# Performance work log

Measured on AMD Instinct MI355X. Metric: run time of the kernel, lower is better.

The kernel has to match this reference:

```python
import jax, jax.numpy as jnp
import numpy as np

N_HOPS = 2
LEAKY_SLOPE = 0.2
EPS = 1e-12


def setup_inputs() -> dict:
    key = jax.random.key(0)
    k1, k2, k3, k4, k5, k6 = jax.random.split(key, 6)
    N, R, C, E = 100000, 50, 64, 1000000
    return {
        "entity_emb": jax.random.normal(k1, (N, C), dtype=jnp.float32) * 0.1,
        "relation_emb": jax.random.normal(k2, (R, C), dtype=jnp.float32) * 0.1,
        "fc_w": jax.random.normal(k3, (C, 2 * C), dtype=jnp.float32) * 0.1,  # torch Linear weight [out, in]
        "fc_b": jax.random.normal(k4, (C,), dtype=jnp.float32) * 0.1,
        "edge_index": jax.random.randint(k5, (2, E), 0, N, dtype=jnp.int64),
        "edge_type": jax.random.randint(k6, (E,), 0, R, dtype=jnp.int64),
    }


def reference(entity_emb, relation_emb, fc_w, fc_b, edge_index, edge_type):
    """RGAT.forward with mess_dropout=False: n_hops of relational-attention
    gather -> leakyrelu -> scatter_softmax(head) -> scatter_sum -> residual -> L2 normalize."""
    N = entity_emb.shape[0]
    head, tail = edge_index[0], edge_index[1]
    rel_e = relation_emb[edge_type]  # [E, C]

    def agg(emb):
        a_input = jnp.concatenate([emb[head], emb[tail]], axis=-1)  # [E, 2C]
        h = a_input @ fc_w.T + fc_b                                  # fc(a_input): [E, C]
        e = jnp.sum(h * rel_e, axis=-1)                              # [E]
        e = jnp.where(e > 0, e, LEAKY_SLOPE * e)                     # leakyrelu(0.2)
        # scatter_softmax over head segments (numerically stable)
        m = jax.ops.segment_max(e, head, num_segments=N)             # [N]
        ex = jnp.exp(e - m[head])
        denom = jax.ops.segment_sum(ex, head, num_segments=N)        # [N]
        w = ex / denom[head]                                         # [E]
        agg_emb = jax.ops.segment_sum(emb[tail] * w[:, None], head, num_segments=N)
        agg_emb = agg_emb + emb                                      # residual
        return agg_emb

    emb = entity_emb
    for _ in range(N_HOPS):
        emb = agg(emb)
        # F.normalize(emb): L2 along dim=1 with eps clamp
        nrm = jnp.sqrt(jnp.sum(emb * emb, axis=-1, keepdims=True))
        emb = emb / jnp.maximum(nrm, EPS)
    return emb
```

## Files before the change

kernel.cpp:

```cpp
#include <hip/hip_runtime.h>

#define C 64
#define RMAX 50
#define LEAKY 0.2f
#define CAP 48

__device__ __forceinline__ float bf2f(unsigned short u) {
  return __uint_as_float(((unsigned)u) << 16);
}
__device__ __forceinline__ unsigned short f2bf(float x) {
  unsigned u = __float_as_uint(x);
  return (unsigned short)((u + 0x7FFFu + ((u >> 16) & 1u)) >> 16);
}

__device__ __forceinline__ int wave_isbf(const void* ent) {
  const unsigned* w = (const unsigned*)ent;
  const int lane = threadIdx.x & 63;
  int ok = 0;
#pragma unroll
  for (int i = 0; i < 4; ++i) {
    unsigned lo = w[lane + 64 * i] & 0xFFFFu;
    float a = fabsf(__uint_as_float(lo << 16));
    ok += (lo == 0u || (a >= 1e-9f && a <= 1e9f)) ? 1 : 0;
  }
#pragma unroll
  for (int d = 1; d < 64; d <<= 1) ok += __shfl_xor(ok, d, 64);
  return ok >= 224;
}
__device__ __forceinline__ int wave_is64(const int* p) {
  const int lane = threadIdx.x & 63;
  int z = (p[2 * lane + 1] == 0) ? 1 : 0;
#pragma unroll
  for (int d = 1; d < 64; d <<= 1) z += __shfl_xor(z, d, 64);
  return z >= 62;
}
__device__ __forceinline__ float loadF(const void* p, int i, int isbf) {
  return isbf ? bf2f(((const unsigned short*)p)[i]) : ((const float*)p)[i];
}

__global__ void uvc_kernel(const void* __restrict__ rel,
                           const void* __restrict__ fcw,
                           const void* __restrict__ fcb,
                           float* __restrict__ U, float* __restrict__ V,
                           float* __restrict__ cvec) {
  const int isbf = wave_isbf(rel);
  const int r = blockIdx.x;
  const int i = threadIdx.x;
  float acc = 0.f;
  for (int o = 0; o < C; ++o)
    acc += loadF(rel, r * C + o, isbf) * loadF(fcw, o * (2 * C) + i, isbf);
  if (i < C) U[r * C + i] = acc;
  else       V[r * C + (i - C)] = acc;
  if (i < C) {
    float p = loadF(rel, r * C + i, isbf) * loadF(fcb, i, isbf);
#pragma unroll
    for (int d = 1; d < 64; d <<= 1) p += __shfl_xor(p, d, 64);
    if (i == 0) cvec[r] = p;
  }
}

__global__ void fillb_kernel(const int* __restrict__ eidx, const int* __restrict__ etype,
                             int* __restrict__ cnt, int* __restrict__ packed,
                             int E, int N, int Rc) {
  const int is64 = wave_is64(eidx);
  const int et64 = wave_is64(etype);
  const int base = (blockIdx.x * blockDim.x + threadIdx.x) * 4;
  int h[4], t[4], r[4];
#pragma unroll
  for (int k = 0; k < 4; ++k) {
    const int e = base + k;
    if (e < E) {
      h[k] = is64 ? eidx[2 * e] : eidx[e];
      t[k] = is64 ? eidx[2 * E + 2 * e] : eidx[E + e];
      r[k] = et64 ? etype[2 * e] : etype[e];
    }
  }
  int pos[4];
#pragma unroll
  for (int k = 0; k < 4; ++k) {
    const int e = base + k;
    if (e < E) {
      if ((unsigned)h[k] >= (unsigned)N) h[k] = 0;
      pos[k] = atomicAdd(&cnt[h[k]], 1);
    }
  }
#pragma unroll
  for (int k = 0; k < 4; ++k) {
    const int e = base + k;
    if (e < E && pos[k] < CAP) {
      int tt = t[k]; if ((unsigned)tt >= (unsigned)N) tt = 0;
      int rr = r[k]; if ((unsigned)rr >= (unsigned)Rc) rr = 0;
      packed[h[k] * CAP + pos[k]] = tt | (rr << 20);
    }
  }
}

__global__ void histo_kernel(const int* __restrict__ cnt, int* __restrict__ hist, int N) {
  __shared__ int histS[65];
  const int tid = threadIdx.x;
  for (int k = tid; k < 65; k += 1024) histS[k] = 0;
  __syncthreads();
  const int i = blockIdx.x * 1024 + tid;
  if (i < N) {
    int b = cnt[i]; if (b > 64) b = 64;
    atomicAdd(&histS[b], 1);
  }
  __syncthreads();
  for (int k = tid; k < 65; k += 1024)
    if (histS[k]) atomicAdd(&hist[k], histS[k]);
}

__global__ void order_kernel(const int* __restrict__ cnt, const int* __restrict__ hist,
                             int* __restrict__ bincur, int* __restrict__ order, int N) {
  __shared__ int binstart[66];
  __shared__ int lh[65];
  __shared__ int lbase[65];
  const int tid = threadIdx.x;
  for (int k = tid; k < 65; k += 1024) { binstart[k] = hist[k]; lh[k] = 0; }
  __syncthreads();
  if (tid == 0) {
    int run = 0;
    for (int k = 0; k < 65; ++k) { int t = binstart[k]; binstart[k] = run; run += t; }
    binstart[65] = run;
  }
  __syncthreads();
  const int i = blockIdx.x * 1024 + tid;
  int b = 0, lpos = 0;
  if (i < N) {
    b = cnt[i]; if (b > 64) b = 64;
    lpos = atomicAdd(&lh[b], 1);
  }
  __syncthreads();
  if (tid < 65) lbase[tid] = lh[tid] ? atomicAdd(&bincur[tid], lh[tid]) : 0;
  __syncthreads();
  if (i < N) {
    int dst = binstart[b] + lbase[b] + lpos;
    if ((unsigned)dst < (unsigned)N) order[dst] = i;
  }
}

__device__ __forceinline__ void unpack8(uint4 u, float4& a, float4& b) {
  a.x = __uint_as_float(u.x << 16); a.y = __uint_as_float(u.x & 0xFFFF0000u);
  a.z = __uint_as_float(u.y << 16); a.w = __uint_as_float(u.y & 0xFFFF0000u);
  b.x = __uint_as_float(u.z << 16); b.y = __uint_as_float(u.z & 0xFFFF0000u);
  b.z = __uint_as_float(u.w << 16); b.w = __uint_as_float(u.w & 0xFFFF0000u);
}

template <bool IN_EXT, bool OUT_EXT>
__global__ __launch_bounds__(256) void hop_kernel(
    const void* __restrict__ emb_in_v, void* __restrict__ emb_out_v,
    const int* __restrict__ cnt, const int* __restrict__ packed,
    const float* __restrict__ Ug, const float* __restrict__ Vg,
    const float* __restrict__ cg, const int* __restrict__ order,
    const void* __restrict__ ent_det, int N, int Rc) {
  const int isbf = wave_isbf(ent_det);
  const int l = threadIdx.x & 7;
  const int slot = blockIdx.x * 32 + (threadIdx.x >> 3);
  if (slot >= N) return;
  const int n = order[slot];

  auto loadRow = [&](int row, float4& a, float4& b) {
    if (IN_EXT && !isbf) {
      const float4* q = (const float4*)((const float*)emb_in_v + (size_t)row * C);
      a = q[2 * l]; b = q[2 * l + 1];
    } else {
      uint4 u = ((const uint4*)emb_in_v)[(size_t)row * 8 + l];
      unpack8(u, a, b);
    }
  };

  const int start = n * CAP;
  int deg = cnt[n];
  if (deg > CAP) deg = CAP;
  if (deg < 0) deg = 0;

  float4 enA, enB;
  loadRow(n, enA, enB);

  float sum = 0.f;
  float4 accA = {0.f, 0.f, 0.f, 0.f}, accB = {0.f, 0.f, 0.f, 0.f};

  float4 etA, etB, uuA, uuB, vvA, vvB;
  float cb = 0.f;
  auto issue = [&](unsigned pkv) {
    int t = (int)(pkv & 0xFFFFFu); if (t >= N) t = 0;
    int r = (int)(pkv >> 20);      if (r >= Rc) r = 0;
    loadRow(t, etA, etB);
    const float4* uq = (const float4*)&Ug[r * C + l * 8];
    const float4* vq = (const float4*)&Vg[r * C + l * 8];
    uuA = uq[0]; uuB = uq[1];
    vvA = vq[0]; vvB = vq[1];
    cb = cg[r];
  };
  if (deg > 0) issue((unsigned)packed[start]);
  int pknext = (deg > 1) ? packed[start + 1] : 0;

  for (int jj = 0; jj < deg; ++jj) {
    const float4 cetA = etA, cetB = etB;
    const float4 cuuA = uuA, cuuB = uuB, cvvA = vvA, cvvB = vvB;
    const float ccb = cb;
    if (jj + 1 < deg) issue((unsigned)pknext);
    if (jj + 2 < deg) pknext = packed[start + jj + 2];

    float p = cuuA.x * enA.x + cuuA.y * enA.y + cuuA.z * enA.z + cuuA.w * enA.w
            + cuuB.x * enB.x + cuuB.y * enB.y + cuuB.z * enB.z + cuuB.w * enB.w
            + cvvA.x * cetA.x + cvvA.y * cetA.y + cvvA.z * cetA.z + cvvA.w * cetA.w
            + cvvB.x * cetB.x + cvvB.y * cetB.y + cvvB.z * cetB.z + cvvB.w * cetB.w;
    p += __shfl_xor(p, 1); p += __shfl_xor(p, 2); p += __shfl_xor(p, 4);
    float s = p + ccb;
    s = s > 0.f ? s : LEAKY * s;
    const float wgt = __expf(fminf(s, 50.f));
    sum += wgt;
    accA.x += wgt * cetA.x; accA.y += wgt * cetA.y;
    accA.z += wgt * cetA.z; accA.w += wgt * cetA.w;
    accB.x += wgt * cetB.x; accB.y += wgt * cetB.y;
    accB.z += wgt * cetB.z; accB.w += wgt * cetB.w;
  }

  const float inv = (deg > 0) ? 1.0f / sum : 0.f;
  float4 oA, oB;
  oA.x = accA.x * inv + enA.x; oA.y = accA.y * inv + enA.y;
  oA.z = accA.z * inv + enA.z; oA.w = accA.w * inv + enA.w;
  oB.x = accB.x * inv + enB.x; oB.y = accB.y * inv + enB.y;
  oB.z = accB.z * inv + enB.z; oB.w = accB.w * inv + enB.w;

  float ss = oA.x * oA.x + oA.y * oA.y + oA.z * oA.z + oA.w * oA.w
           + oB.x * oB.x + oB.y * oB.y + oB.z * oB.z + oB.w * oB.w;
  ss += __shfl_xor(ss, 1); ss += __shfl_xor(ss, 2); ss += __shfl_xor(ss, 4);
  const float sc = 1.0f / fmaxf(sqrtf(ss), 1e-12f);
  oA.x *= sc; oA.y *= sc; oA.z *= sc; oA.w *= sc;
  oB.x *= sc; oB.y *= sc; oB.z *= sc; oB.w *= sc;

  if (OUT_EXT && !isbf) {
    float4* q = (float4*)((float*)emb_out_v + (size_t)n * C);
    q[2 * l] = oA; q[2 * l + 1] = oB;
  } else {
    uint4 u;
    u.x = (unsigned)f2bf(oA.x) | ((unsigned)f2bf(oA.y) << 16);
    u.y = (unsigned)f2bf(oA.z) | ((unsigned)f2bf(oA.w) << 16);
    u.z = (unsigned)f2bf(oB.x) | ((unsigned)f2bf(oB.y) << 16);
    u.w = (unsigned)f2bf(oB.z) | ((unsigned)f2bf(oB.w) << 16);
    ((uint4*)emb_out_v)[(size_t)n * 8 + l] = u;
  }
}

extern "C" void kernel_launch(void* const* d_in, const int* in_sizes, int n_in,
                              void* d_out, int out_size, void* d_ws, size_t ws_size,
                              hipStream_t stream) {
  const void* ent  = d_in[0];
  const void* rel  = d_in[1];
  const void* fcw  = d_in[2];
  const void* fcb  = d_in[3];
  const int* eidx  = (const int*)d_in[4];
  const int* etype = (const int*)d_in[5];

  const int N  = in_sizes[0] / C;
  const int R0 = in_sizes[1] / C;
  const int Rc = R0 < RMAX ? R0 : RMAX;
  const int E  = in_sizes[5];
  const int nbN = (N + 1023) / 1024;
  (void)n_in; (void)out_size; (void)ws_size;

  char* ws = (char*)d_ws;
  size_t off = 0;
  auto alloc = [&](size_t bytes) -> void* {
    void* p = ws + off;
    off = (off + bytes + 255) & ~(size_t)255;
    return p;
  };
  int*   cnt    = (int*)alloc(((size_t)N + 256) * 4);
  int*   hist   = cnt + N;
  int*   bincur = hist + 128;
  float* U      = (float*)alloc((size_t)Rc * C * 4);
  float* V      = (float*)alloc((size_t)Rc * C * 4);
  float* cv     = (float*)alloc((size_t)Rc * 4);
  int*   order  = (int*)alloc((size_t)N * 4);
  int*   packed = (int*)alloc((size_t)N * CAP * 4);
  unsigned short* mid = (unsigned short*)alloc((size_t)N * C * 2);

  hipMemsetAsync(cnt, 0, ((size_t)N + 256) * 4, stream);
  uvc_kernel<<<Rc, 128, 0, stream>>>(rel, fcw, fcb, U, V, cv);
  fillb_kernel<<<(E + 1023) / 1024, 256, 0, stream>>>(eidx, etype, cnt, packed, E, N, Rc);
  histo_kernel<<<nbN, 1024, 0, stream>>>(cnt, hist, N);
  order_kernel<<<nbN, 1024, 0, stream>>>(cnt, hist, bincur, order, N);

  const int hb = (N + 31) / 32;
  hop_kernel<true,  false><<<hb, 256, 0, stream>>>(ent, mid,   cnt, packed, U, V, cv, order, ent, N, Rc);
  hop_kernel<false, true ><<<hb, 256, 0, stream>>>(mid, d_out, cnt, packed, U, V, cv, order, ent, N, Rc);
}
```

Baseline: 259.8 us.

## Bucket edges by head before CSR fill and pre-convert input embeddings to bf16

Edge bucketing now runs in two passes. The first pass groups edges into coarse head-range buckets using shared-memory counters. The second pass fills the per-node packed adjacency bucket by bucket, which localizes the global atomics and scattered writes. A new conversion kernel turns the fp32 entity embeddings into bf16 before hop 1, so the first hop's gathers read half the bytes. Both paths depend on having enough workspace, fall back to the old code otherwise, and add extra kernels and memory traffic for the staging buffers.

```diff
diff --git a/kernel.cpp b/kernel.cpp
--- a/kernel.cpp
+++ b/kernel.cpp
@@ -59,6 +59,25 @@
   }
 }
 
+__global__ void conv_kernel(const void* __restrict__ ent, unsigned* __restrict__ dst,
+                            int n8) {
+  const int isbf = wave_isbf(ent);
+  int i = blockIdx.x * blockDim.x + threadIdx.x;
+  if (i >= n8) return;
+  uint4 o;
+  if (isbf) {
+    o = ((const uint4*)ent)[i];
+  } else {
+    const float4* q = (const float4*)ent;
+    float4 a = q[2 * i], b = q[2 * i + 1];
+    o.x = (unsigned)f2bf(a.x) | ((unsigned)f2bf(a.y) << 16);
+    o.y = (unsigned)f2bf(a.z) | ((unsigned)f2bf(a.w) << 16);
+    o.z = (unsigned)f2bf(b.x) | ((unsigned)f2bf(b.y) << 16);
+    o.w = (unsigned)f2bf(b.z) | ((unsigned)f2bf(b.w) << 16);
+  }
+  ((uint4*)dst)[i] = o;
+}
+
 __global__ void fillb_kernel(const int* __restrict__ eidx, const int* __restrict__ etype,
                              int* __restrict__ cnt, int* __restrict__ packed,
                              int E, int N, int Rc) {
@@ -95,6 +114,60 @@
   }
 }
 
+__global__ void fillA_kernel(const int* __restrict__ eidx, const int* __restrict__ etype,
+                             int* __restrict__ bcnt, int2* __restrict__ bbuf,
+                             int E, int N, int Rc, int shift, int nbuck, int bcap) {
+  __shared__ int lh[256];
+  __shared__ int gbase[256];
+  const int is64 = wave_is64(eidx);
+  const int et64 = wave_is64(etype);
+  const int tid = threadIdx.x;
+  if (tid < 256) lh[tid] = 0;
+  const int eBase = blockIdx.x * 2048;
+  int h[8], tr[8], bk[8], lp[8], ok[8];
+  __syncthreads();
+#pragma unroll
+  for (int k = 0; k < 8; ++k) {
+    const int e = eBase + k * 256 + tid;
+    ok[k] = (e < E);
+    if (ok[k]) {
+      int hh = is64 ? eidx[2 * e] : eidx[e];
+      int tt = is64 ? eidx[2 * E + 2 * e] : eidx[E + e];
+      int rr = et64 ? etype[2 * e] : etype[e];
+      if ((unsigned)hh >= (unsigned)N) hh = 0;
+      if ((unsigned)tt >= (unsigned)N) tt = 0;
+      if ((unsigned)rr >= (unsigned)Rc) rr = 0;
+      h[k] = hh; tr[k] = tt | (rr << 20);
+      bk[k] = hh >> shift;
+      lp[k] = atomicAdd(&lh[bk[k]], 1);
+    }
+  }
+  __syncthreads();
+  if (tid < nbuck) gbase[tid] = lh[tid] ? atomicAdd(&bcnt[tid], lh[tid]) : 0;
+  __syncthreads();
+#pragma unroll
+  for (int k = 0; k < 8; ++k) {
+    if (ok[k]) {
+      int posb = gbase[bk[k]] + lp[k];
+      if (posb < bcap) bbuf[(size_t)bk[k] * bcap + posb] = make_int2(h[k], tr[k]);
+    }
+  }
+}
+
+__global__ void fillB_kernel(const int* __restrict__ bcnt, const int2* __restrict__ bbuf,
+                             int* __restrict__ cnt, int* __restrict__ packed,
+                             int N, int bcap) {
+  const int b = blockIdx.x;
+  int bc = bcnt[b]; if (bc > bcap) bc = bcap;
+  const int2* src = &bbuf[(size_t)b * bcap];
+  for (int k = threadIdx.x; k < bc; k += blockDim.x) {
+    int2 e = src[k];
+    int h = e.x; if ((unsigned)h >= (unsigned)N) h = 0;
+    int pos = atomicAdd(&cnt[h], 1);
+    if (pos < CAP) packed[h * CAP + pos] = e.y;
+  }
+}
+
 __global__ void histo_kernel(const int* __restrict__ cnt, int* __restrict__ hist, int N) {
   __shared__ int histS[65];
   const int tid = threadIdx.x;
@@ -153,7 +226,8 @@
     const float* __restrict__ Ug, const float* __restrict__ Vg,
     const float* __restrict__ cg, const int* __restrict__ order,
     const void* __restrict__ ent_det, int N, int Rc) {
-  const int isbf = wave_isbf(ent_det);
+  int isbf = 1;
+  if (IN_EXT || OUT_EXT) isbf = wave_isbf(ent_det);
   const int l = threadIdx.x & 7;
   const int slot = blockIdx.x * 32 + (threadIdx.x >> 3);
   if (slot >= N) return;
@@ -259,7 +333,13 @@
   const int Rc = R0 < RMAX ? R0 : RMAX;
   const int E  = in_sizes[5];
   const int nbN = (N + 1023) / 1024;
-  (void)n_in; (void)out_size; (void)ws_size;
+  (void)n_in; (void)out_size;
+
+  int shift = 9;
+  while ((((N - 1) >> shift) + 1) > 256) shift++;
+  const int nbuck = ((N - 1) >> shift) + 1;
+  int bcap = (E + nbuck - 1) / nbuck;
+  bcap += bcap / 4 + 256;
 
   char* ws = (char*)d_ws;
   size_t off = 0;
@@ -268,23 +348,49 @@
     off = (off + bytes + 255) & ~(size_t)255;
     return p;
   };
-  int*   cnt    = (int*)alloc(((size_t)N + 256) * 4);
+  int*   cnt    = (int*)alloc(((size_t)N + 512) * 4);
   int*   hist   = cnt + N;
   int*   bincur = hist + 128;
+  int*   bcnt   = bincur + 128;
   float* U      = (float*)alloc((size_t)Rc * C * 4);
   float* V      = (float*)alloc((size_t)Rc * C * 4);
   float* cv     = (float*)alloc((size_t)Rc * 4);
   int*   order  = (int*)alloc((size_t)N * 4);
   int*   packed = (int*)alloc((size_t)N * CAP * 4);
-  unsigned short* mid = (unsigned short*)alloc((size_t)N * C * 2);
-
-  hipMemsetAsync(cnt, 0, ((size_t)N + 256) * 4, stream);
+  const size_t emb0B   = (size_t)N * C * 2;
+  const size_t bucketB = (size_t)nbuck * bcap * 8;
+  const size_t midB    = (size_t)N * C * 2;
+  const size_t base    = off;
+  const size_t align = 256;
+  const bool tier2 = base + ((emb0B > bucketB ? emb0B : bucketB) + align) + (midB + align) <= ws_size;
+  const bool tier1 = base + (emb0B + align) + (midB + align) <= ws_size;
+
+  void* unionbuf = alloc(tier2 ? (emb0B > bucketB ? emb0B : bucketB)
+                                : (tier1 ? emb0B : 0));
+  unsigned short* mid = (unsigned short*)alloc(midB);
+  unsigned short* emb0 = (unsigned short*)unionbuf;
+  int2* bbuf = (int2*)unionbuf;
+
+  hipMemsetAsync(cnt, 0, ((size_t)N + 512) * 4, stream);
   uvc_kernel<<<Rc, 128, 0, stream>>>(rel, fcw, fcb, U, V, cv);
-  fillb_kernel<<<(E + 1023) / 1024, 256, 0, stream>>>(eidx, etype, cnt, packed, E, N, Rc);
+
+  if (tier2) {
+    fillA_kernel<<<(E + 2047) / 2048, 256, 0, stream>>>(eidx, etype, bcnt, bbuf,
+                                                        E, N, Rc, shift, nbuck, bcap);
+    fillB_kernel<<<nbuck, 256, 0, stream>>>(bcnt, bbuf, cnt, packed, N, bcap);
+  } else {
+    fillb_kernel<<<(E + 1023) / 1024, 256, 0, stream>>>(eidx, etype, cnt, packed, E, N, Rc);
+  }
   histo_kernel<<<nbN, 1024, 0, stream>>>(cnt, hist, N);
   order_kernel<<<nbN, 1024, 0, stream>>>(cnt, hist, bincur, order, N);
 
   const int hb = (N + 31) / 32;
-  hop_kernel<true,  false><<<hb, 256, 0, stream>>>(ent, mid,   cnt, packed, U, V, cv, order, ent, N, Rc);
+  if (tier1 || tier2) {
+    const int n8 = N * C / 8;
+    conv_kernel<<<(n8 + 255) / 256, 256, 0, stream>>>(ent, (unsigned*)emb0, n8);
+    hop_kernel<false, false><<<hb, 256, 0, stream>>>(emb0, mid, cnt, packed, U, V, cv, order, ent, N, Rc);
+  } else {
+    hop_kernel<true,  false><<<hb, 256, 0, stream>>>(ent, mid, cnt, packed, U, V, cv, order, ent, N, Rc);
+  }
   hop_kernel<false, true ><<<hb, 256, 0, stream>>>(mid, d_out, cnt, packed, U, V, cv, order, ent, N, Rc);
 }
```

Result: faster. 242.0 us (-6.9%).
